# Performance work log

Hardware: AMD Instinct MI355X
Metric: run time of the kernel (lower is better)

Reference implementation:

```python
import jax, jax.numpy as jnp
import numpy as np

B, C = 4194304, 6
DEMI = C // 2            # demi_len = preds.shape[1] / 2
THRESH = 0.65            # confidence threshold from the original loop
PENALTY_WEIGHT = 0.1


def setup_inputs() -> dict:
    key = jax.random.key(0)
    k1, k2 = jax.random.split(key)
    preds = jax.random.normal(k1, (B, C), dtype=jnp.float32)
    labels = jax.random.randint(k2, (B,), 0, C)
    targets = jax.nn.one_hot(labels, C, dtype=jnp.float32)  # CE with probability targets
    return {"preds": preds, "targets": targets}


def reference(preds, targets):
    # base_loss: torch.nn.CrossEntropyLoss with probability targets, mean reduction
    logp = jax.nn.log_softmax(preds, axis=-1)
    base_loss = -jnp.mean(jnp.sum(targets * logp, axis=-1))

    # --- vectorized replica of the per-row Python loop ---
    s = jax.nn.sigmoid(preds)
    sR, sL = s[:, :DEMI], s[:, DEMI:]
    maxR = jnp.max(sR, axis=1)
    idxR = jnp.argmax(sR, axis=1)
    maxL = jnp.max(sL, axis=1)
    idxL = jnp.argmax(sL, axis=1)

    r_set = maxR > THRESH
    l_set = maxL > THRESH
    none_set = (~r_set) & (~l_set)
    r_wins = maxR > maxL  # strict >, else-branch picks left (matches original)

    useR = (r_set | (none_set & r_wins)).astype(jnp.float32)
    useL = (l_set | (none_set & ~r_wins)).astype(jnp.float32)

    pvR = jax.nn.one_hot(idxR, DEMI, dtype=jnp.float32) * useR[:, None]
    pvL = jax.nn.one_hot(idxL, DEMI, dtype=jnp.float32) * useL[:, None]
    # if both halves exceed threshold, row sums to 2 -> divided by its sum (0.5 each)
    both = r_set & l_set
    scale = jnp.where(both, 0.5, 1.0)[:, None]
    pv = jnp.concatenate([pvR, pvL], axis=1) * scale  # [B, 6]

    # penalty: original uses hardcoded :3 / 3: splits and whole-batch target sums
    t_left = jnp.sum(targets[:, :3]) > 0
    t_right = jnp.sum(targets[:, 3:]) > 0
    left_fn = (jnp.sum(pv[:, :3], axis=1) == 0) & t_left
    # right check reads prediction_vector[:, 3:].sum() at iteration j, i.e. rows 0..j
    right_cum = jnp.cumsum(jnp.sum(pv[:, 3:], axis=1))
    right_fn = (right_cum == 0) & t_right
    penalty_fn = jnp.sum((left_fn | right_fn).astype(jnp.float32))

    # penalty is a Python float in the original -> constant w.r.t. autodiff
    penalty = PENALTY_WEIGHT * penalty_fn
    return base_loss + jax.lax.stop_gradient(penalty)
```

## Files before the change

kernel.cpp:

```cpp
#include <hip/hip_runtime.h>
#include <climits>

static constexpr float kLogitThresh = 0.61903920840622351f;
static constexpr int NB = 2048;

__device__ __forceinline__ void row_op(
    const float p[6], const float t[6], int row,
    float& lossSum, int& cnt, int& minK, int& tl, int& tr) {
  float mR = fmaxf(fmaxf(p[0], p[1]), p[2]);
  float mL = fmaxf(fmaxf(p[3], p[4]), p[5]);
  bool rs = mR > kLogitThresh;
  bool ls = mL > kLogitThresh;
  bool none = (!rs) && (!ls);
  bool rwins = mR > mL;
  bool useR = rs || (none && rwins);
  bool useL = ls || (none && !rwins);
  if (!useR) cnt++;
  if (useL && row < minK) minK = row;
  float tsumL = t[0] + t[1] + t[2];
  float tsumR = t[3] + t[4] + t[5];
  if (tsumL > 0.0f) tl = 1;
  if (tsumR > 0.0f) tr = 1;
  float m = fmaxf(mR, mL);
  float se = 0.0f, tp = 0.0f, ts = 0.0f;
#pragma unroll
  for (int j = 0; j < 6; ++j) {
    se += __expf(p[j] - m);
    tp += t[j] * p[j];
    ts += t[j];
  }
  float lse = m + __logf(se);
  lossSum += lse * ts - tp;
}

__global__ __launch_bounds__(256) void loss_main(
    const float4* __restrict__ gp, const float4* __restrict__ gt,
    int nGroups,
    float* __restrict__ pLoss, int* __restrict__ pCnt,
    int* __restrict__ pMinK, int* __restrict__ pTl, int* __restrict__ pTr) {
  int tid = blockIdx.x * blockDim.x + threadIdx.x;
  int stride = gridDim.x * blockDim.x;
  float lossSum = 0.0f;
  int cnt = 0;
  int minK = INT_MAX;
  int tl = 0, tr = 0;

  for (int g = tid; g < nGroups; g += stride) {
    size_t base = (size_t)g * 6;
    float4 a0 = gp[base + 0];
    float4 a1 = gp[base + 1];
    float4 a2 = gp[base + 2];
    float4 a3 = gp[base + 3];
    float4 a4 = gp[base + 4];
    float4 a5 = gp[base + 5];
    float4 b0 = gt[base + 0];
    float4 b1 = gt[base + 1];
    float4 b2 = gt[base + 2];
    float4 b3 = gt[base + 3];
    float4 b4 = gt[base + 4];
    float4 b5 = gt[base + 5];
    int row0 = 4 * g;
    {
      float p[6] = {a0.x, a0.y, a0.z, a0.w, a1.x, a1.y};
      float t[6] = {b0.x, b0.y, b0.z, b0.w, b1.x, b1.y};
      row_op(p, t, row0, lossSum, cnt, minK, tl, tr);
    }
    {
      float p[6] = {a1.z, a1.w, a2.x, a2.y, a2.z, a2.w};
      float t[6] = {b1.z, b1.w, b2.x, b2.y, b2.z, b2.w};
      row_op(p, t, row0 + 1, lossSum, cnt, minK, tl, tr);
    }
    {
      float p[6] = {a3.x, a3.y, a3.z, a3.w, a4.x, a4.y};
      float t[6] = {b3.x, b3.y, b3.z, b3.w, b4.x, b4.y};
      row_op(p, t, row0 + 2, lossSum, cnt, minK, tl, tr);
    }
    {
      float p[6] = {a4.z, a4.w, a5.x, a5.y, a5.z, a5.w};
      float t[6] = {b4.z, b4.w, b5.x, b5.y, b5.z, b5.w};
      row_op(p, t, row0 + 3, lossSum, cnt, minK, tl, tr);
    }
  }

#pragma unroll
  for (int off = 32; off > 0; off >>= 1) {
    lossSum += __shfl_down(lossSum, off);
    cnt     += __shfl_down(cnt, off);
    minK    = min(minK, __shfl_down(minK, off));
    tl      |= __shfl_down(tl, off);
    tr      |= __shfl_down(tr, off);
  }

  __shared__ float wLoss[4];
  __shared__ int wCnt[4], wMinK[4], wTl[4], wTr[4];
  int wave = threadIdx.x >> 6;
  int lane = threadIdx.x & 63;
  if (lane == 0) {
    wLoss[wave] = lossSum; wCnt[wave] = cnt; wMinK[wave] = minK;
    wTl[wave] = tl; wTr[wave] = tr;
  }
  __syncthreads();
  if (threadIdx.x == 0) {
    pLoss[blockIdx.x] = wLoss[0] + wLoss[1] + wLoss[2] + wLoss[3];
    pCnt[blockIdx.x]  = wCnt[0] + wCnt[1] + wCnt[2] + wCnt[3];
    pMinK[blockIdx.x] = min(min(wMinK[0], wMinK[1]), min(wMinK[2], wMinK[3]));
    pTl[blockIdx.x]   = wTl[0] | wTl[1] | wTl[2] | wTl[3];
    pTr[blockIdx.x]   = wTr[0] | wTr[1] | wTr[2] | wTr[3];
  }
}

__global__ __launch_bounds__(1024) void reduce_final(
    const float* __restrict__ pLoss, const int* __restrict__ pCnt,
    const int* __restrict__ pMinK, const int* __restrict__ pTl,
    const int* __restrict__ pTr, float* __restrict__ out, int B) {
  int tid = threadIdx.x;
  double L = 0.0;
  int cnt = 0, mk = INT_MAX, tl = 0, tr = 0;
#pragma unroll
  for (int r = 0; r < NB / 1024; ++r) {
    int i = tid + r * 1024;
    L   += (double)pLoss[i];
    cnt += pCnt[i];
    mk   = min(mk, pMinK[i]);
    tl  |= pTl[i];
    tr  |= pTr[i];
  }
#pragma unroll
  for (int off = 32; off > 0; off >>= 1) {
    L   += __shfl_down(L, off);
    cnt += __shfl_down(cnt, off);
    mk   = min(mk, __shfl_down(mk, off));
    tl  |= __shfl_down(tl, off);
    tr  |= __shfl_down(tr, off);
  }
  __shared__ double sL[16];
  __shared__ int sC[16], sM[16], sT[16], sR[16];
  int wave = tid >> 6;
  int lane = tid & 63;
  if (lane == 0) {
    sL[wave] = L; sC[wave] = cnt; sM[wave] = mk; sT[wave] = tl; sR[wave] = tr;
  }
  __syncthreads();
  if (tid == 0) {
    double Lt = 0.0;
    int Cn = 0, K = INT_MAX, Tl = 0, Tr = 0;
#pragma unroll
    for (int w = 0; w < 16; ++w) {
      Lt += sL[w]; Cn += sC[w]; K = min(K, sM[w]); Tl |= sT[w]; Tr |= sR[w];
    }
    if (K > B) K = B;
    double base = Lt / (double)B;
    double pen = 0.1 * ((Tl ? (double)Cn : 0.0) + (Tr ? (double)K : 0.0));
    out[0] = (float)(base + pen);
  }
}

extern "C" void kernel_launch(void* const* d_in, const int* in_sizes, int n_in,
                              void* d_out, int out_size, void* d_ws, size_t ws_size,
                              hipStream_t stream) {
  const float4* preds   = (const float4*)d_in[0];
  const float4* targets = (const float4*)d_in[1];
  float* out = (float*)d_out;

  float* pLoss = (float*)d_ws;
  int*   pCnt  = (int*)((char*)d_ws + NB * 4);
  int*   pMinK = (int*)((char*)d_ws + NB * 8);
  int*   pTl   = (int*)((char*)d_ws + NB * 12);
  int*   pTr   = (int*)((char*)d_ws + NB * 16);

  int B = in_sizes[0] / 6;
  int nGroups = B / 4;

  hipLaunchKernelGGL(loss_main, dim3(NB), dim3(256), 0, stream,
                     preds, targets, nGroups, pLoss, pCnt, pMinK, pTl, pTr);
  hipLaunchKernelGGL(reduce_final, dim3(1), dim3(1024), 0, stream,
                     pLoss, pCnt, pMinK, pTl, pTr, out, B);
}
```

Baseline: 38.91 us.

## Fuse final reduction into main kernel via hierarchical last-block atomic counters

Removes the separate single-block reduce kernel and instead has the last block to finish (found through a two-level atomic counter tree of 32 groups) perform the final reduction. The aim is to drop one kernel launch and its launch gap. In exchange it adds a memset of the counters on every call, threadfences, and atomics per block. The memset is itself another stream operation, so launch overhead may not shrink much.

After: 106.2 us. +172.8%, slower.

```diff
diff --git a/kernel.cpp b/kernel.cpp
--- a/kernel.cpp
+++ b/kernel.cpp
@@ -3,6 +3,8 @@
 
 static constexpr float kLogitThresh = 0.61903920840622351f;
 static constexpr int NB = 2048;
+static constexpr int NGRP = 32;
+static constexpr int CTR_OFF = 65536;
 
 __device__ __forceinline__ void row_op(
     const float p[6], const float t[6], int row,
@@ -33,11 +35,13 @@
   lossSum += lse * ts - tp;
 }
 
-__global__ __launch_bounds__(256) void loss_main(
+__global__ __launch_bounds__(256) void loss_fused(
     const float4* __restrict__ gp, const float4* __restrict__ gt,
     int nGroups,
     float* __restrict__ pLoss, int* __restrict__ pCnt,
-    int* __restrict__ pMinK, int* __restrict__ pTl, int* __restrict__ pTr) {
+    int* __restrict__ pMinK, int* __restrict__ pTl, int* __restrict__ pTr,
+    unsigned int* __restrict__ ctrBase,
+    float* __restrict__ out, int B) {
   int tid = blockIdx.x * blockDim.x + threadIdx.x;
   int stride = gridDim.x * blockDim.x;
   float lossSum = 0.0f;
@@ -100,58 +104,63 @@
     wTl[wave] = tl; wTr[wave] = tr;
   }
   __syncthreads();
+
+  __shared__ int sLast;
   if (threadIdx.x == 0) {
     pLoss[blockIdx.x] = wLoss[0] + wLoss[1] + wLoss[2] + wLoss[3];
     pCnt[blockIdx.x]  = wCnt[0] + wCnt[1] + wCnt[2] + wCnt[3];
     pMinK[blockIdx.x] = min(min(wMinK[0], wMinK[1]), min(wMinK[2], wMinK[3]));
     pTl[blockIdx.x]   = wTl[0] | wTl[1] | wTl[2] | wTl[3];
     pTr[blockIdx.x]   = wTr[0] | wTr[1] | wTr[2] | wTr[3];
-  }
-}
 
-__global__ __launch_bounds__(1024) void reduce_final(
-    const float* __restrict__ pLoss, const int* __restrict__ pCnt,
-    const int* __restrict__ pMinK, const int* __restrict__ pTl,
-    const int* __restrict__ pTr, float* __restrict__ out, int B) {
-  int tid = threadIdx.x;
-  double L = 0.0;
-  int cnt = 0, mk = INT_MAX, tl = 0, tr = 0;
-#pragma unroll
-  for (int r = 0; r < NB / 1024; ++r) {
-    int i = tid + r * 1024;
-    L   += (double)pLoss[i];
-    cnt += pCnt[i];
-    mk   = min(mk, pMinK[i]);
-    tl  |= pTl[i];
-    tr  |= pTr[i];
-  }
-#pragma unroll
-  for (int off = 32; off > 0; off >>= 1) {
-    L   += __shfl_down(L, off);
-    cnt += __shfl_down(cnt, off);
-    mk   = min(mk, __shfl_down(mk, off));
-    tl  |= __shfl_down(tl, off);
-    tr  |= __shfl_down(tr, off);
-  }
-  __shared__ double sL[16];
-  __shared__ int sC[16], sM[16], sT[16], sR[16];
-  int wave = tid >> 6;
-  int lane = tid & 63;
-  if (lane == 0) {
-    sL[wave] = L; sC[wave] = cnt; sM[wave] = mk; sT[wave] = tl; sR[wave] = tr;
+    __threadfence();
+    int last = 0;
+    unsigned int* gc = ctrBase + (blockIdx.x & (NGRP - 1)) * 32;
+    if (atomicAdd(gc, 1u) == (NB / NGRP) - 1) {
+      if (atomicAdd(ctrBase + NGRP * 32, 1u) == NGRP - 1) last = 1;
+    }
+    sLast = last;
   }
   __syncthreads();
-  if (tid == 0) {
-    double Lt = 0.0;
-    int Cn = 0, K = INT_MAX, Tl = 0, Tr = 0;
+
+  if (sLast) {
+    __threadfence();
+    double L = 0.0;
+    int c2 = 0, mk = INT_MAX, l2 = 0, r2 = 0;
 #pragma unroll
-    for (int w = 0; w < 16; ++w) {
-      Lt += sL[w]; Cn += sC[w]; K = min(K, sM[w]); Tl |= sT[w]; Tr |= sR[w];
+    for (int r = 0; r < NB / 256; ++r) {
+      int i = threadIdx.x + r * 256;
+      L  += (double)pLoss[i];
+      c2 += pCnt[i];
+      mk  = min(mk, pMinK[i]);
+      l2 |= pTl[i];
+      r2 |= pTr[i];
     }
-    if (K > B) K = B;
-    double base = Lt / (double)B;
-    double pen = 0.1 * ((Tl ? (double)Cn : 0.0) + (Tr ? (double)K : 0.0));
-    out[0] = (float)(base + pen);
+#pragma unroll
+    for (int off = 32; off > 0; off >>= 1) {
+      L  += __shfl_down(L, off);
+      c2 += __shfl_down(c2, off);
+      mk  = min(mk, __shfl_down(mk, off));
+      l2 |= __shfl_down(l2, off);
+      r2 |= __shfl_down(r2, off);
+    }
+    __shared__ double sL[4];
+    __shared__ int sC[4], sM[4], sT[4], sR[4];
+    if (lane == 0) {
+      sL[wave] = L; sC[wave] = c2; sM[wave] = mk; sT[wave] = l2; sR[wave] = r2;
+    }
+    __syncthreads();
+    if (threadIdx.x == 0) {
+      double Lt = sL[0] + sL[1] + sL[2] + sL[3];
+      int Cn = sC[0] + sC[1] + sC[2] + sC[3];
+      int K  = min(min(sM[0], sM[1]), min(sM[2], sM[3]));
+      int Tl = sT[0] | sT[1] | sT[2] | sT[3];
+      int Tr = sR[0] | sR[1] | sR[2] | sR[3];
+      if (K > B) K = B;
+      double base = Lt / (double)B;
+      double pen = 0.1 * ((Tl ? (double)Cn : 0.0) + (Tr ? (double)K : 0.0));
+      out[0] = (float)(base + pen);
+    }
   }
 }
 
@@ -167,12 +176,14 @@
   int*   pMinK = (int*)((char*)d_ws + NB * 8);
   int*   pTl   = (int*)((char*)d_ws + NB * 12);
   int*   pTr   = (int*)((char*)d_ws + NB * 16);
+  unsigned int* ctr = (unsigned int*)((char*)d_ws + CTR_OFF);
 
   int B = in_sizes[0] / 6;
   int nGroups = B / 4;
 
-  hipLaunchKernelGGL(loss_main, dim3(NB), dim3(256), 0, stream,
-                     preds, targets, nGroups, pLoss, pCnt, pMinK, pTl, pTr);
-  hipLaunchKernelGGL(reduce_final, dim3(1), dim3(1024), 0, stream,
-                     pLoss, pCnt, pMinK, pTl, pTr, out, B);
+  hipMemsetAsync(ctr, 0, (NGRP + 1) * 128, stream);
+
+  hipLaunchKernelGGL(loss_fused, dim3(NB), dim3(256), 0, stream,
+                     preds, targets, nGroups,
+                     pLoss, pCnt, pMinK, pTl, pTr, ctr, out, B);
 }
```
